# Kernel optimization log

Hardware: AMD Instinct MI355X
Metric: run time of the kernel (lower is better)

Reference implementation:

```python
import jax, jax.numpy as jnp
import numpy as np

OBS_LEN = 8
PRED_LEN = 12
BATCH = 65536
EMB = 64
H = 64


def setup_inputs() -> dict:
    key = jax.random.key(0)
    ks = jax.random.split(key, 18)
    s = 1.0 / np.sqrt(H)  # torch default uniform bound scale, used as std here

    def p(k, shape):
        return (jax.random.normal(k, shape, dtype=jnp.float32) * s).astype(jnp.float32)

    return {
        "obs_traj": jax.random.normal(ks[0], (OBS_LEN, BATCH, 2), dtype=jnp.float32),
        "obs_traj_rel": jax.random.normal(ks[1], (OBS_LEN, BATCH, 2), dtype=jnp.float32),
        # encoder params
        "enc_emb_w": p(ks[2], (EMB, 2)),
        "enc_emb_b": p(ks[3], (EMB,)),
        "enc_w_ih": p(ks[4], (4 * H, EMB)),
        "enc_w_hh": p(ks[5], (4 * H, H)),
        "enc_b_ih": p(ks[6], (4 * H,)),
        "enc_b_hh": p(ks[7], (4 * H,)),
        # decoder params
        "dec_emb_w": p(ks[8], (EMB, 2)),
        "dec_emb_b": p(ks[9], (EMB,)),
        "dec_w_ih": p(ks[10], (4 * H, EMB)),
        "dec_w_hh": p(ks[11], (4 * H, H)),
        "dec_b_ih": p(ks[12], (4 * H,)),
        "dec_b_hh": p(ks[13], (4 * H,)),
        "h2p_w": p(ks[14], (2, H)),
        "h2p_b": p(ks[15], (2,)),
    }


def _lstm_cell(h, c, x, w_ih, w_hh, b_ih, b_hh):
    # torch nn.LSTM gate order: i, f, g, o
    gates = x @ w_ih.T + h @ w_hh.T + (b_ih + b_hh)
    i, f, g, o = jnp.split(gates, 4, axis=-1)
    c_new = jax.nn.sigmoid(f) * c + jax.nn.sigmoid(i) * jnp.tanh(g)
    h_new = jax.nn.sigmoid(o) * jnp.tanh(c_new)
    return h_new, c_new


def reference(obs_traj, obs_traj_rel,
              enc_emb_w, enc_emb_b, enc_w_ih, enc_w_hh, enc_b_ih, enc_b_hh,
              dec_emb_w, dec_emb_b, dec_w_ih, dec_w_hh, dec_b_ih, dec_b_hh,
              h2p_w, h2p_b):
    batch = obs_traj_rel.shape[1]

    # ---------- Encoder ----------
    enc_in = obs_traj_rel @ enc_emb_w.T + enc_emb_b  # [T, B, EMB]

    def enc_step(carry, x_t):
        h, c = carry
        h, c = _lstm_cell(h, c, x_t, enc_w_ih, enc_w_hh, enc_b_ih, enc_b_hh)
        return (h, c), None

    h0 = jnp.zeros((batch, H), dtype=obs_traj_rel.dtype)
    c0 = jnp.zeros((batch, H), dtype=obs_traj_rel.dtype)
    (h_enc, _), _ = jax.lax.scan(enc_step, (h0, c0), enc_in)

    # ---------- Decoder ----------
    dec_h = h_enc                                   # final encoder hidden seeds decoder
    dec_c = jnp.zeros((batch, H), dtype=obs_traj_rel.dtype)
    last_pos_rel = obs_traj_rel[-1]
    dec_in = last_pos_rel @ dec_emb_w.T + dec_emb_b  # [B, EMB]

    def dec_step(carry, _):
        h, c, x = carry
        h, c = _lstm_cell(h, c, x, dec_w_ih, dec_w_hh, dec_b_ih, dec_b_hh)
        rel_pos = h @ h2p_w.T + h2p_b               # [B, 2]
        x_next = rel_pos @ dec_emb_w.T + dec_emb_b  # [B, EMB]
        return (h, c, x_next), rel_pos

    (_, _, _), pred_traj_fake_rel = jax.lax.scan(
        dec_step, (dec_h, dec_c, dec_in), None, length=PRED_LEN)
    return pred_traj_fake_rel  # [PRED_LEN, B, 2]
```

## Files before the change

### kernel.cpp

```cpp
#include <hip/hip_runtime.h>

#define OBS_LEN 8
#define PRED_LEN 12
#define TILE_B 32
#define NTHREADS 256

typedef __attribute__((ext_vector_type(8))) short short8;
typedef __attribute__((ext_vector_type(4))) float floatx4;
typedef __attribute__((ext_vector_type(2))) float floatx2;
typedef __attribute__((ext_vector_type(2))) unsigned int u32x2;
typedef unsigned short u16;
typedef unsigned int u32;

#define L2E 1.442695040888963f

__device__ __forceinline__ u16 f2bf(float f) {
  __bf16 b = (__bf16)f;
  return __builtin_bit_cast(u16, b);
}
__device__ __forceinline__ float bf2f(u16 h) {
  return __builtin_bit_cast(float, ((u32)h) << 16);
}
__device__ __forceinline__ float rndbf(float f) { return (float)(__bf16)f; }

#if __has_builtin(__builtin_amdgcn_exp2f)
__device__ __forceinline__ float fexp2_(float x) { return __builtin_amdgcn_exp2f(x); }
#else
__device__ __forceinline__ float fexp2_(float x) { return exp2f(x); }
#endif
__device__ __forceinline__ floatx2 exp2v(floatx2 x) {
  floatx2 r;
  r.x = fexp2_(x.x);
  r.y = fexp2_(x.y);
  return r;
}
#if __has_builtin(__builtin_amdgcn_rcpf)
__device__ __forceinline__ floatx2 rcp2(floatx2 x) {
  floatx2 r;
  r.x = __builtin_amdgcn_rcpf(x.x);
  r.y = __builtin_amdgcn_rcpf(x.y);
  return r;
}
#else
__device__ __forceinline__ floatx2 rcp2(floatx2 x) {
  return floatx2{1.0f / x.x, 1.0f / x.y};
}
#endif

__device__ __forceinline__ floatx4 mfma_bf(short8 a, short8 b, floatx4 c) {
  return __builtin_amdgcn_mfma_f32_16x16x32_bf16(a, b, c, 0, 0, 0);
}

__device__ __forceinline__ int swz(int s, int b) {
  return s * 64 + ((b ^ (s & 7)) * 8);
}

__device__ __forceinline__ void load_afrags(const float* __restrict__ W,
                                            short8 (&af)[4][2],
                                            int u0, int q, int l16) {
#pragma unroll
  for (int t = 0; t < 4; ++t)
#pragma unroll
    for (int kf = 0; kf < 2; ++kf) {
      const float* src = W + (t * 64 + u0 + l16) * 64 + kf * 32 + q * 8;
      const floatx4 w0 = *(const floatx4*)src;
      const floatx4 w1 = *(const floatx4*)(src + 4);
      short8 a;
#pragma unroll
      for (int j = 0; j < 4; ++j) {
        a[j] = (short)f2bf(w0[j]);
        a[j + 4] = (short)f2bf(w1[j]);
      }
      af[t][kf] = a;
    }
}

__device__ __forceinline__ void load_afrags_eff(const float* __restrict__ Whh,
                                                const float* __restrict__ aS0,
                                                const float* __restrict__ aS1,
                                                const float* __restrict__ hw0,
                                                const float* __restrict__ hw1,
                                                short8 (&af)[4][2],
                                                int u0, int q, int l16) {
#pragma unroll
  for (int t = 0; t < 4; ++t) {
    const int g = t * 64 + u0 + l16;
    const float a0 = aS0[g], a1 = aS1[g];
#pragma unroll
    for (int kf = 0; kf < 2; ++kf) {
      const int u = kf * 32 + q * 8;
      const float* src = Whh + g * 64 + u;
      const floatx4 w0 = *(const floatx4*)src;
      const floatx4 w1 = *(const floatx4*)(src + 4);
      const floatx4 p00 = *(const floatx4*)(hw0 + u);
      const floatx4 p01 = *(const floatx4*)(hw0 + u + 4);
      const floatx4 p10 = *(const floatx4*)(hw1 + u);
      const floatx4 p11 = *(const floatx4*)(hw1 + u + 4);
      short8 a;
#pragma unroll
      for (int j = 0; j < 4; ++j) {
        a[j] = (short)f2bf(w0[j] + a0 * p00[j] + a1 * p10[j]);
        a[j + 4] = (short)f2bf(w1[j] + a0 * p01[j] + a1 * p11[j]);
      }
      af[t][kf] = a;
    }
  }
}

__device__ __forceinline__ void nonlin_store(const floatx4 (&acc)[4],
                                             floatx2 (&c2)[2],
                                             u16* __restrict__ wrh,
                                             int s, int q, int wv) {
  const int sw = s & 7;
  u32 hpk[2];
#pragma unroll
  for (int p = 0; p < 2; ++p) {
    const floatx2 iv = {acc[0][2 * p], acc[0][2 * p + 1]};
    const floatx2 fv = {acc[1][2 * p], acc[1][2 * p + 1]};
    const floatx2 gv = {acc[2][2 * p], acc[2][2 * p + 1]};
    const floatx2 ov = {acc[3][2 * p], acc[3][2 * p + 1]};
    const floatx2 ei = exp2v(iv * -L2E);
    const floatx2 ef = exp2v(fv * -L2E);
    const floatx2 eg = exp2v(gv * (2.0f * L2E));
    const floatx2 eo = exp2v(ov * -L2E);
    const floatx2 A = ei + 1.0f;
    const floatx2 F = ef + 1.0f;
    const floatx2 Bg = eg + 1.0f;
    const floatx2 P = A * Bg;
    const floatx2 num = c2[p] * P + (eg - 1.0f) * F;
    const floatx2 cn = num * rcp2(F * P);
    c2[p] = cn;
    const floatx2 ec = exp2v(cn * (2.0f * L2E));
    const floatx2 h = (ec - 1.0f) * rcp2((eo + 1.0f) * (ec + 1.0f));
    hpk[p] = (u32)f2bf(h.x) | ((u32)f2bf(h.y) << 16);
  }
  *(u32x2*)(wrh + s * 64 + (((wv * 2 + (q >> 1)) ^ sw) * 8) + (q & 1) * 4) =
      u32x2{hpk[0], hpk[1]};
}

__device__ __forceinline__ void cell_step(const u16* __restrict__ rdh,
                                          const u16* __restrict__ rdx,
                                          u16* __restrict__ wrh,
                                          const short8 (&afh)[4][2],
                                          const short8 (&afx)[4][2],
                                          const float* __restrict__ biasrow,
                                          floatx2 (&c)[2][2],
                                          int q, int l16, int wv, int u0) {
#pragma unroll
  for (int n = 0; n < 2; ++n) {
    const int s = n * 16 + l16;
    const int sw = s & 7;
    const u16* hr = rdh + s * 64;
    const u16* xr = rdx + s * 64;
    const short8 hb0 = *(const short8*)(hr + ((q ^ sw) * 8));
    const short8 hb1 = *(const short8*)(hr + (((q + 4) ^ sw) * 8));
    const short8 xb0 = *(const short8*)(xr + ((q ^ sw) * 8));
    const short8 xb1 = *(const short8*)(xr + (((q + 4) ^ sw) * 8));
    floatx4 acc[4];
#pragma unroll
    for (int t = 0; t < 4; ++t) {
      const floatx4 bias = *(const floatx4*)(biasrow + t * 64 + u0 + q * 4);
      acc[t] = mfma_bf(afh[t][0], hb0, bias);
    }
#pragma unroll
    for (int t = 0; t < 4; ++t) acc[t] = mfma_bf(afx[t][0], xb0, acc[t]);
#pragma unroll
    for (int t = 0; t < 4; ++t) acc[t] = mfma_bf(afh[t][1], hb1, acc[t]);
#pragma unroll
    for (int t = 0; t < 4; ++t) acc[t] = mfma_bf(afx[t][1], xb1, acc[t]);
    nonlin_store(acc, c[n], wrh, s, q, wv);
  }
}

__device__ __forceinline__ void dec_step_folded(
    const u16* __restrict__ rdh, u16* __restrict__ wrh,
    const short8 (&af)[4][2], const float* __restrict__ biasrow,
    const float* __restrict__ hw0, const float* __restrict__ hw1,
    float b2p0, float b2p1, float* __restrict__ outp, long S0,
    floatx2 (&c)[2][2], int q, int l16, int wv, int u0) {
  short8 hb0[2], hb1[2];
#pragma unroll
  for (int n = 0; n < 2; ++n) {
    const int s = n * 16 + l16, sw = s & 7;
    const u16* hr = rdh + s * 64;
    hb0[n] = *(const short8*)(hr + ((q ^ sw) * 8));
    hb1[n] = *(const short8*)(hr + (((q + 4) ^ sw) * 8));
  }
  floatx4 acc[2][4];
#pragma unroll
  for (int t = 0; t < 4; ++t) {
    const floatx4 bias = *(const floatx4*)(biasrow + t * 64 + u0 + q * 4);
    acc[0][t] = mfma_bf(af[t][0], hb0[0], bias);
    acc[1][t] = mfma_bf(af[t][0], hb0[1], bias);
  }
#pragma unroll
  for (int t = 0; t < 4; ++t) {
    acc[0][t] = mfma_bf(af[t][1], hb1[0], acc[0][t]);
    acc[1][t] = mfma_bf(af[t][1], hb1[1], acc[1][t]);
  }
  floatx2 d[2] = {floatx2{0.f, 0.f}, floatx2{0.f, 0.f}};
#pragma unroll
  for (int hf = 0; hf < 2; ++hf) {
    const int ub = hf * 32 + q * 8;
    const floatx4 wa0 = *(const floatx4*)(hw0 + ub);
    const floatx4 wa1 = *(const floatx4*)(hw0 + ub + 4);
    const floatx4 wb0 = *(const floatx4*)(hw1 + ub);
    const floatx4 wb1 = *(const floatx4*)(hw1 + ub + 4);
#pragma unroll
    for (int n = 0; n < 2; ++n) {
      const short8 hb = hf ? hb1[n] : hb0[n];
#pragma unroll
      for (int j = 0; j < 4; ++j) {
        const float h0 = bf2f((u16)hb[j]);
        const float h1 = bf2f((u16)hb[j + 4]);
        d[n].x += wa0[j] * h0 + wa1[j] * h1;
        d[n].y += wb0[j] * h0 + wb1[j] * h1;
      }
    }
  }
#pragma unroll
  for (int n = 0; n < 2; ++n) {
    d[n].x += __shfl_xor(d[n].x, 16);
    d[n].x += __shfl_xor(d[n].x, 32);
    d[n].y += __shfl_xor(d[n].y, 16);
    d[n].y += __shfl_xor(d[n].y, 32);
  }
  if (q == 0) {
#pragma unroll
    for (int n = 0; n < 2; ++n)
      *(floatx2*)(outp + (S0 + n * 16 + l16) * 2) =
          floatx2{d[n].x + b2p0, d[n].y + b2p1};
  }
#pragma unroll
  for (int n = 0; n < 2; ++n)
    nonlin_store(acc[n], c[n], wrh, n * 16 + l16, q, wv);
}

__device__ __forceinline__ void rel_only(const u16* __restrict__ rdh,
                                         const float* __restrict__ hw0,
                                         const float* __restrict__ hw1,
                                         float b2p0, float b2p1,
                                         float* __restrict__ outp, long S0,
                                         int q, int l16) {
  floatx2 d[2] = {floatx2{0.f, 0.f}, floatx2{0.f, 0.f}};
#pragma unroll
  for (int n = 0; n < 2; ++n) {
    const int s = n * 16 + l16, sw = s & 7;
    const u16* hr = rdh + s * 64;
    const short8 hb0 = *(const short8*)(hr + ((q ^ sw) * 8));
    const short8 hb1 = *(const short8*)(hr + (((q + 4) ^ sw) * 8));
#pragma unroll
    for (int hf = 0; hf < 2; ++hf) {
      const int ub = hf * 32 + q * 8;
      const floatx4 wa0 = *(const floatx4*)(hw0 + ub);
      const floatx4 wa1 = *(const floatx4*)(hw0 + ub + 4);
      const floatx4 wb0 = *(const floatx4*)(hw1 + ub);
      const floatx4 wb1 = *(const floatx4*)(hw1 + ub + 4);
      const short8 hb = hf ? hb1 : hb0;
#pragma unroll
      for (int j = 0; j < 4; ++j) {
        const float h0 = bf2f((u16)hb[j]);
        const float h1 = bf2f((u16)hb[j + 4]);
        d[n].x += wa0[j] * h0 + wa1[j] * h1;
        d[n].y += wb0[j] * h0 + wb1[j] * h1;
      }
    }
  }
#pragma unroll
  for (int n = 0; n < 2; ++n) {
    d[n].x += __shfl_xor(d[n].x, 16);
    d[n].x += __shfl_xor(d[n].x, 32);
    d[n].y += __shfl_xor(d[n].y, 16);
    d[n].y += __shfl_xor(d[n].y, 32);
  }
  if (q == 0) {
#pragma unroll
    for (int n = 0; n < 2; ++n)
      *(floatx2*)(outp + (S0 + n * 16 + l16) * 2) =
          floatx2{d[n].x + b2p0, d[n].y + b2p1};
  }
}

__device__ __forceinline__ void xgen8(float rb0, float rb1,
                                      const float* __restrict__ ew0,
                                      const float* __restrict__ ew1,
                                      const float* __restrict__ eb,
                                      u16* __restrict__ xw, int s8, int p8) {
  short8 v;
#pragma unroll
  for (int j = 0; j < 8; ++j) {
    const int e = p8 * 8 + j;
    v[j] = (short)f2bf(rb0 * ew0[e] + (rb1 * ew1[e] + eb[e]));
  }
  *(short8*)(xw + swz(s8, p8)) = v;
}

__global__ void __launch_bounds__(NTHREADS, 3)
lstm_kernel(const float* __restrict__ obs_rel,
            const float* __restrict__ enc_emb_w, const float* __restrict__ enc_emb_b,
            const float* __restrict__ enc_w_ih, const float* __restrict__ enc_w_hh,
            const float* __restrict__ enc_b_ih, const float* __restrict__ enc_b_hh,
            const float* __restrict__ dec_emb_w, const float* __restrict__ dec_emb_b,
            const float* __restrict__ dec_w_ih, const float* __restrict__ dec_w_hh,
            const float* __restrict__ dec_b_ih, const float* __restrict__ dec_b_hh,
            const float* __restrict__ h2p_w, const float* __restrict__ h2p_b,
            float* __restrict__ out, int batch) {
  __shared__ __align__(16) u16 hS[2][TILE_B * 64];
  __shared__ __align__(16) u16 xS[2][TILE_B * 64];
  __shared__ __align__(16) float posS[OBS_LEN][TILE_B * 2];
  __shared__ __align__(16) float biasS[3][256];
  __shared__ float ew0e[64], ew1e[64], ebe[64];
  __shared__ float ew0d[64], ew1d[64], ebd[64];
  __shared__ __align__(16) float aS0[256], aS1[256];
  __shared__ __align__(16) float hw0S[64], hw1S[64];

  const int tid = threadIdx.x;
  const int wv = tid >> 6, lane = tid & 63;
  const int q = lane >> 4, l16 = lane & 15;
  const int u0 = wv << 4;
  const int s8 = tid >> 3, p8 = tid & 7;
  const long S0 = (long)blockIdx.x * TILE_B;

  if (tid < 128) {
    const int t = tid >> 4, i = tid & 15;
    *(floatx4*)&posS[t][i * 4] =
        *(const floatx4*)(obs_rel + (long)t * batch * 2 + S0 * 2 + i * 4);
  }
  if (tid < 64) {
    ew0e[tid] = rndbf(enc_emb_w[tid * 2]);
    ew1e[tid] = rndbf(enc_emb_w[tid * 2 + 1]);
    ebe[tid] = enc_emb_b[tid];
    ew0d[tid] = rndbf(dec_emb_w[tid * 2]);
    ew1d[tid] = rndbf(dec_emb_w[tid * 2 + 1]);
    ebd[tid] = dec_emb_b[tid];
    hw0S[tid] = h2p_w[tid];
    hw1S[tid] = h2p_w[64 + tid];
  }
  biasS[0][tid] = enc_b_ih[tid] + enc_b_hh[tid];
  {
    float A0 = 0.f, A1 = 0.f, B0 = 0.f;
    const float* wr = dec_w_ih + tid * 64;
#pragma unroll
    for (int e4 = 0; e4 < 16; ++e4) {
      const floatx4 w = *(const floatx4*)(wr + e4 * 4);
      const floatx4 m0 = *(const floatx4*)(dec_emb_w + e4 * 8);
      const floatx4 m1 = *(const floatx4*)(dec_emb_w + e4 * 8 + 4);
      const floatx4 bb = *(const floatx4*)(dec_emb_b + e4 * 4);
      A0 += w[0] * m0[0] + w[1] * m0[2] + w[2] * m1[0] + w[3] * m1[2];
      A1 += w[0] * m0[1] + w[1] * m0[3] + w[2] * m1[1] + w[3] * m1[3];
      B0 += w[0] * bb[0] + w[1] * bb[1] + w[2] * bb[2] + w[3] * bb[3];
    }
    aS0[tid] = A0;
    aS1[tid] = A1;
    const float db = dec_b_ih[tid] + dec_b_hh[tid];
    biasS[1][tid] = db;
    biasS[2][tid] = db + B0 + A0 * h2p_b[0] + A1 * h2p_b[1];
  }
  for (int i = tid; i < TILE_B * 64 / 2; i += NTHREADS) ((u32*)&hS[0][0])[i] = 0;

  short8 afh[4][2], afx[4][2];
  floatx2 c[2][2];
  load_afrags(enc_w_hh, afh, u0, q, l16);
  load_afrags(enc_w_ih, afx, u0, q, l16);
  c[0][0] = c[0][1] = c[1][0] = c[1][1] = floatx2{0.f, 0.f};
  const float b2p0 = h2p_b[0], b2p1 = h2p_b[1];
  __syncthreads();
  {
    const floatx2 rr = *(const floatx2*)(&posS[0][s8 * 2]);
    xgen8(rndbf(rr.x), rndbf(rr.y), ew0e, ew1e, ebe, xS[0], s8, p8);
  }
  __syncthreads();

  int pb = 0;
#pragma unroll 1
  for (int t = 0; t < OBS_LEN; ++t) {
    const int tn = t + 1;
    const floatx2 rr = *(const floatx2*)(&posS[(tn < 8) ? tn : 7][s8 * 2]);
    if (tn < 8)
      xgen8(rndbf(rr.x), rndbf(rr.y), ew0e, ew1e, ebe, xS[tn & 1], s8, p8);
    else
      xgen8(rndbf(rr.x), rndbf(rr.y), ew0d, ew1d, ebd, xS[0], s8, p8);
    cell_step(hS[pb], xS[t & 1], hS[pb ^ 1], afh, afx, &biasS[0][0], c,
              q, l16, wv, u0);
    __syncthreads();
    pb ^= 1;
  }

  load_afrags(dec_w_hh, afh, u0, q, l16);
  load_afrags(dec_w_ih, afx, u0, q, l16);
  c[0][0] = c[0][1] = c[1][0] = c[1][1] = floatx2{0.f, 0.f};
  cell_step(hS[pb], xS[0], hS[pb ^ 1], afh, afx, &biasS[1][0], c,
            q, l16, wv, u0);
  load_afrags_eff(dec_w_hh, aS0, aS1, hw0S, hw1S, afh, u0, q, l16);
  __syncthreads();
  pb ^= 1;

#pragma unroll 1
  for (int j = 1; j < PRED_LEN; ++j) {
    dec_step_folded(hS[pb], hS[pb ^ 1], afh, &biasS[2][0], hw0S, hw1S,
                    b2p0, b2p1, out + (long)(j - 1) * batch * 2, S0, c,
                    q, l16, wv, u0);
    __syncthreads();
    pb ^= 1;
  }

  rel_only(hS[pb], hw0S, hw1S, b2p0, b2p1,
           out + (long)(PRED_LEN - 1) * batch * 2, S0, q, l16);
}

extern "C" void kernel_launch(void* const* d_in, const int* in_sizes, int n_in,
                              void* d_out, int out_size, void* d_ws, size_t ws_size,
                              hipStream_t stream) {
  const float* obs_rel = (const float*)d_in[1];
  const int batch = in_sizes[1] / (OBS_LEN * 2);

  const int blocks = batch / TILE_B;
  hipLaunchKernelGGL(lstm_kernel, dim3(blocks), dim3(NTHREADS), 0, stream,
                     obs_rel,
                     (const float*)d_in[2], (const float*)d_in[3],
                     (const float*)d_in[4], (const float*)d_in[5],
                     (const float*)d_in[6], (const float*)d_in[7],
                     (const float*)d_in[8], (const float*)d_in[9],
                     (const float*)d_in[10], (const float*)d_in[11],
                     (const float*)d_in[12], (const float*)d_in[13],
                     (const float*)d_in[14], (const float*)d_in[15],
                     (float*)d_out, batch);
}
```

Baseline: 233.0 us.

## Compute h2p projection with MFMA and stage decoder outputs in LDS

The per-step hidden-to-position projection was a scalar FMA loop with cross-lane shuffles run by every wave. It now uses two bf16 MFMA instructions on waves 0-1, with the h2p weights packed into an A-fragment whose rows 0 and 1 hold the two output channels. Outputs are kept in a shared-memory buffer and written to global memory with coalesced stores at the end. This removes redundant VALU and shuffle work from the serial decoder loop. In exchange the projection weights are rounded to bf16, and the extra LDS buffer may reduce occupancy.

```diff
diff --git a/kernel.cpp b/kernel.cpp
--- a/kernel.cpp
+++ b/kernel.cpp
@@ -174,9 +174,9 @@
 
 __device__ __forceinline__ void dec_step_folded(
     const u16* __restrict__ rdh, u16* __restrict__ wrh,
-    const short8 (&af)[4][2], const float* __restrict__ biasrow,
-    const float* __restrict__ hw0, const float* __restrict__ hw1,
-    float b2p0, float b2p1, float* __restrict__ outp, long S0,
+    const short8 (&af)[4][2], const short8 (&afp)[2],
+    const float* __restrict__ biasrow, float b2p0, float b2p1,
+    float* __restrict__ relrow,
     floatx2 (&c)[2][2], int q, int l16, int wv, int u0) {
   short8 hb0[2], hb1[2];
 #pragma unroll
@@ -198,87 +198,18 @@
     acc[0][t] = mfma_bf(af[t][1], hb1[0], acc[0][t]);
     acc[1][t] = mfma_bf(af[t][1], hb1[1], acc[1][t]);
   }
-  floatx2 d[2] = {floatx2{0.f, 0.f}, floatx2{0.f, 0.f}};
-#pragma unroll
-  for (int hf = 0; hf < 2; ++hf) {
-    const int ub = hf * 32 + q * 8;
-    const floatx4 wa0 = *(const floatx4*)(hw0 + ub);
-    const floatx4 wa1 = *(const floatx4*)(hw0 + ub + 4);
-    const floatx4 wb0 = *(const floatx4*)(hw1 + ub);
-    const floatx4 wb1 = *(const floatx4*)(hw1 + ub + 4);
-#pragma unroll
-    for (int n = 0; n < 2; ++n) {
-      const short8 hb = hf ? hb1[n] : hb0[n];
-#pragma unroll
-      for (int j = 0; j < 4; ++j) {
-        const float h0 = bf2f((u16)hb[j]);
-        const float h1 = bf2f((u16)hb[j + 4]);
-        d[n].x += wa0[j] * h0 + wa1[j] * h1;
-        d[n].y += wb0[j] * h0 + wb1[j] * h1;
-      }
-    }
-  }
-#pragma unroll
-  for (int n = 0; n < 2; ++n) {
-    d[n].x += __shfl_xor(d[n].x, 16);
-    d[n].x += __shfl_xor(d[n].x, 32);
-    d[n].y += __shfl_xor(d[n].y, 16);
-    d[n].y += __shfl_xor(d[n].y, 32);
-  }
-  if (q == 0) {
-#pragma unroll
-    for (int n = 0; n < 2; ++n)
-      *(floatx2*)(outp + (S0 + n * 16 + l16) * 2) =
-          floatx2{d[n].x + b2p0, d[n].y + b2p1};
+  if (wv < 2) {
+    const short8 ha = wv ? hb0[1] : hb0[0];
+    const short8 hc = wv ? hb1[1] : hb1[0];
+    floatx4 ar = mfma_bf(afp[0], ha, floatx4{0.f, 0.f, 0.f, 0.f});
+    ar = mfma_bf(afp[1], hc, ar);
+    if (q == 0)
+      *(floatx2*)(relrow + (wv * 16 + l16) * 2) =
+          floatx2{ar[0] + b2p0, ar[1] + b2p1};
   }
 #pragma unroll
   for (int n = 0; n < 2; ++n)
     nonlin_store(acc[n], c[n], wrh, n * 16 + l16, q, wv);
-}
-
-__device__ __forceinline__ void rel_only(const u16* __restrict__ rdh,
-                                         const float* __restrict__ hw0,
-                                         const float* __restrict__ hw1,
-                                         float b2p0, float b2p1,
-                                         float* __restrict__ outp, long S0,
-                                         int q, int l16) {
-  floatx2 d[2] = {floatx2{0.f, 0.f}, floatx2{0.f, 0.f}};
-#pragma unroll
-  for (int n = 0; n < 2; ++n) {
-    const int s = n * 16 + l16, sw = s & 7;
-    const u16* hr = rdh + s * 64;
-    const short8 hb0 = *(const short8*)(hr + ((q ^ sw) * 8));
-    const short8 hb1 = *(const short8*)(hr + (((q + 4) ^ sw) * 8));
-#pragma unroll
-    for (int hf = 0; hf < 2; ++hf) {
-      const int ub = hf * 32 + q * 8;
-      const floatx4 wa0 = *(const floatx4*)(hw0 + ub);
-      const floatx4 wa1 = *(const floatx4*)(hw0 + ub + 4);
-      const floatx4 wb0 = *(const floatx4*)(hw1 + ub);
-      const floatx4 wb1 = *(const floatx4*)(hw1 + ub + 4);
-      const short8 hb = hf ? hb1 : hb0;
-#pragma unroll
-      for (int j = 0; j < 4; ++j) {
-        const float h0 = bf2f((u16)hb[j]);
-        const float h1 = bf2f((u16)hb[j + 4]);
-        d[n].x += wa0[j] * h0 + wa1[j] * h1;
-        d[n].y += wb0[j] * h0 + wb1[j] * h1;
-      }
-    }
-  }
-#pragma unroll
-  for (int n = 0; n < 2; ++n) {
-    d[n].x += __shfl_xor(d[n].x, 16);
-    d[n].x += __shfl_xor(d[n].x, 32);
-    d[n].y += __shfl_xor(d[n].y, 16);
-    d[n].y += __shfl_xor(d[n].y, 32);
-  }
-  if (q == 0) {
-#pragma unroll
-    for (int n = 0; n < 2; ++n)
-      *(floatx2*)(outp + (S0 + n * 16 + l16) * 2) =
-          floatx2{d[n].x + b2p0, d[n].y + b2p1};
-  }
 }
 
 __device__ __forceinline__ void xgen8(float rb0, float rb1,
@@ -313,6 +244,7 @@
   __shared__ float ew0d[64], ew1d[64], ebd[64];
   __shared__ __align__(16) float aS0[256], aS1[256];
   __shared__ __align__(16) float hw0S[64], hw1S[64];
+  __shared__ __align__(16) float relS[PRED_LEN][TILE_B * 2];
 
   const int tid = threadIdx.x;
   const int wv = tid >> 6, lane = tid & 63;
@@ -392,20 +324,51 @@
   cell_step(hS[pb], xS[0], hS[pb ^ 1], afh, afx, &biasS[1][0], c,
             q, l16, wv, u0);
   load_afrags_eff(dec_w_hh, aS0, aS1, hw0S, hw1S, afh, u0, q, l16);
+  short8 afp[2];
+#pragma unroll
+  for (int kf = 0; kf < 2; ++kf) {
+    const int kb = kf * 32 + q * 8;
+    short8 a;
+#pragma unroll
+    for (int j = 0; j < 4; ++j) {
+      const float r0 = (l16 == 0) ? hw0S[kb + j] : (l16 == 1) ? hw1S[kb + j] : 0.f;
+      const float r1 =
+          (l16 == 0) ? hw0S[kb + 4 + j] : (l16 == 1) ? hw1S[kb + 4 + j] : 0.f;
+      a[j] = (short)f2bf(r0);
+      a[j + 4] = (short)f2bf(r1);
+    }
+    afp[kf] = a;
+  }
   __syncthreads();
   pb ^= 1;
 
 #pragma unroll 1
   for (int j = 1; j < PRED_LEN; ++j) {
-    dec_step_folded(hS[pb], hS[pb ^ 1], afh, &biasS[2][0], hw0S, hw1S,
-                    b2p0, b2p1, out + (long)(j - 1) * batch * 2, S0, c,
-                    q, l16, wv, u0);
+    dec_step_folded(hS[pb], hS[pb ^ 1], afh, afp, &biasS[2][0], b2p0, b2p1,
+                    &relS[j - 1][0], c, q, l16, wv, u0);
     __syncthreads();
     pb ^= 1;
   }
 
-  rel_only(hS[pb], hw0S, hw1S, b2p0, b2p1,
-           out + (long)(PRED_LEN - 1) * batch * 2, S0, q, l16);
+  if (wv < 2) {
+    const int s = wv * 16 + l16, sw = s & 7;
+    const u16* hr = hS[pb] + s * 64;
+    const short8 ha = *(const short8*)(hr + ((q ^ sw) * 8));
+    const short8 hc = *(const short8*)(hr + (((q + 4) ^ sw) * 8));
+    floatx4 ar = mfma_bf(afp[0], ha, floatx4{0.f, 0.f, 0.f, 0.f});
+    ar = mfma_bf(afp[1], hc, ar);
+    if (q == 0)
+      *(floatx2*)(&relS[PRED_LEN - 1][s * 2]) =
+          floatx2{ar[0] + b2p0, ar[1] + b2p1};
+  }
+  __syncthreads();
+
+#pragma unroll
+  for (int r = 0; r < 3; ++r) {
+    const int f = tid + r * 256;
+    const int j = f >> 6, e = f & 63;
+    out[(long)j * batch * 2 + S0 * 2 + e] = ((const float*)relS)[f];
+  }
 }
 
 extern "C" void kernel_launch(void* const* d_in, const int* in_sizes, int n_in,
```

Result: faster. 218.5 us (-6.2%).
